# Performance work log

Hardware: AMD Instinct MI355X
Metric: run time of the kernel (lower is better)

Reference implementation:

```python
import jax, jax.numpy as jnp
import numpy as np

N = 50000      # nodes
E = 800000     # edges
IN = 256       # in_dim
D = 64         # hidden_dim per head
H = 4          # heads
OUT = 40       # out_dim (classes)
SLOPE = 0.2    # leaky relu negative slope


def _gat_conv(h, src, dst, W, al, ar, heads, dh, res=None, act=False):
    """DGL-style GATConv. h:[N,Fin], W:[Fin,heads*dh], al/ar:[heads,dh]."""
    n = h.shape[0]
    feat = (h @ W).reshape(n, heads, dh)                 # [N,H,D]
    el = jnp.sum(feat * al, axis=-1)                     # [N,H]
    er = jnp.sum(feat * ar, axis=-1)                     # [N,H]
    e = jax.nn.leaky_relu(el[src] + er[dst], SLOPE)      # [E,H]
    # segment softmax over incoming edges of each dst node
    m = jax.ops.segment_max(e, dst, num_segments=n)      # [N,H]
    ex = jnp.exp(e - m[dst])                             # [E,H]
    s = jax.ops.segment_sum(ex, dst, num_segments=n)     # [N,H]
    alpha = ex / s[dst]                                  # [E,H]
    rst = jax.ops.segment_sum(alpha[:, :, None] * feat[src], dst, num_segments=n)  # [N,H,D]
    if res is not None:
        rst = rst + res
    if act:
        rst = jax.nn.elu(rst)
    return rst


def setup_inputs():
    key = jax.random.key(0)
    ks = jax.random.split(key, 16)
    def p(k, shape, fan_in):
        return (jax.random.normal(k, shape, jnp.float32) / np.sqrt(fan_in)).astype(jnp.float32)
    inputs = jax.random.normal(ks[0], (N, IN), jnp.float32)
    src = jax.random.randint(ks[1], (E,), 0, N, dtype=jnp.int32)
    dst = jax.random.randint(ks[2], (E,), 0, N, dtype=jnp.int32)
    return {
        "inputs": inputs, "src": src, "dst": dst,
        "W0": p(ks[3], (IN, H * D), IN), "al0": p(ks[4], (H, D), D), "ar0": p(ks[5], (H, D), D),
        "W1": p(ks[6], (H * D, H * D), H * D), "al1": p(ks[7], (H, D), D), "ar1": p(ks[8], (H, D), D),
        "Wo": p(ks[9], (H * D, H * OUT), H * D), "alo": p(ks[10], (H, OUT), OUT), "aro": p(ks[11], (H, OUT), OUT),
        "res_Wo": p(ks[12], (H * D, H * OUT), H * D),
        "fc_W": p(ks[13], (IN, D), IN),
    }


def reference(inputs, src, dst, W0, al0, ar0, W1, al1, ar1, Wo, alo, aro, res_Wo, fc_W):
    # layer 0: no residual, elu activation
    h = _gat_conv(inputs, src, dst, W0, al0, ar0, H, D, res=None, act=True)
    h = h.reshape(N, H * D)
    # layer 1: identity residual (in_feats == heads*out_feats), elu
    res1 = h.reshape(N, H, D)
    h = _gat_conv(h, src, dst, W1, al1, ar1, H, D, res=res1, act=True)
    h = h.reshape(N, H * D)
    # output layer: linear residual projection, no activation, mean over heads
    res_o = (h @ res_Wo).reshape(N, H, OUT)
    logits = _gat_conv(h, src, dst, Wo, alo, aro, H, OUT, res=res_o, act=False).mean(axis=1)
    seq_fts = inputs @ fc_W
    return (logits, h, seq_fts)
```

## Files before the change

### kernel.cpp

```cpp
#include <hip/hip_runtime.h>

typedef unsigned short u16;
typedef unsigned int u32;
typedef __attribute__((ext_vector_type(8))) short short8;
typedef __attribute__((ext_vector_type(4))) float f32x4;

#define NN 50000
#define EE 800000
#define EPAD (EE + 8*NN)

__device__ __forceinline__ float b2f(u16 u){ union{float f;u32 i;}x; x.i=((u32)u)<<16; return x.f; }
__device__ __forceinline__ u16 f2b(float f){ union{float f;u32 i;}x; x.f=f; u32 i=x.i; return (u16)((i + 0x7fffu + ((i>>16)&1u))>>16); }

__global__ void k_f2b4(const float* __restrict__ x, u16* __restrict__ y, int n4){
  int i = blockIdx.x*256 + threadIdx.x;
  if (i >= n4) return;
  float4 v = ((const float4*)x)[i];
  ushort4 o; o.x=f2b(v.x); o.y=f2b(v.y); o.z=f2b(v.z); o.w=f2b(v.w);
  ((ushort4*)y)[i]=o;
}

__global__ void k_wtr(const float* __restrict__ W, u16* __restrict__ Wt, int N){
  int i = blockIdx.x*256 + threadIdx.x;
  if (i >= 256*N) return;
  int k = i / N, n = i % N;
  Wt[(size_t)n*256 + k] = f2b(W[i]);
}

__global__ void k_catWoT(const float* __restrict__ rWo, const float* __restrict__ Wo, u16* __restrict__ Bct){
  int i = blockIdx.x*256 + threadIdx.x;
  if (i >= 256*320) return;
  int k = i/320, c = i%320;
  float v = (c < 160) ? rWo[k*160 + c] : Wo[k*160 + (c-160)];
  Bct[(size_t)c*256 + k] = f2b(v);
}

__global__ void k_count(const int* __restrict__ dst, int* __restrict__ cnt){
  int i = blockIdx.x*256+threadIdx.x; if (i<EE) atomicAdd(&cnt[dst[i]],1);
}

__global__ void k_scan_blocks(const int* __restrict__ cnt, int* __restrict__ off, int* __restrict__ part, int n){
  __shared__ int ts[256];
  int t = threadIdx.x; int base = blockIdx.x*1024 + t*4;
  int c0 = (base+0<n)?((cnt[base+0]+7)&~7):0;
  int c1 = (base+1<n)?((cnt[base+1]+7)&~7):0;
  int c2 = (base+2<n)?((cnt[base+2]+7)&~7):0;
  int c3 = (base+3<n)?((cnt[base+3]+7)&~7):0;
  int s = c0+c1+c2+c3;
  ts[t]=s; __syncthreads();
  for (int d=1; d<256; d<<=1){ int v=(t>=d)?ts[t-d]:0; __syncthreads(); ts[t]+=v; __syncthreads(); }
  int ex = ts[t]-s;
  if (t==255) part[blockIdx.x]=ts[255];
  if (base+0<n) off[base+0]=ex; ex+=c0;
  if (base+1<n) off[base+1]=ex; ex+=c1;
  if (base+2<n) off[base+2]=ex; ex+=c2;
  if (base+3<n) off[base+3]=ex;
}

__global__ void k_scan_part(int* part, int nb){
  if (threadIdx.x==0 && blockIdx.x==0){ int run=0; for(int i=0;i<nb;++i){ int v=part[i]; part[i]=run; run+=v; } }
}

__global__ void k_addback(int* off, int* cur, const int* __restrict__ part, int n){
  int base = blockIdx.x*1024 + threadIdx.x*4; int p = part[blockIdx.x];
  #pragma unroll
  for (int j=0;j<4;++j) if (base+j<n){ int v = off[base+j]+p; off[base+j]=v; if (base+j<NN) cur[base+j]=v; }
}

__global__ void k_scatter(const int* __restrict__ src, const int* __restrict__ dst, int* __restrict__ cur,
                          int* __restrict__ srcs){
  int i = blockIdx.x*256+threadIdx.x; if (i>=EE) return;
  int d = dst[i]; int p = atomicAdd(&cur[d],1);
  srcs[p]=src[i];
}

template<int BN, int MODE>
__global__ __launch_bounds__(256) void k_gemm2(const u16* __restrict__ A, const u16* __restrict__ Bt,
                                               void* __restrict__ C0, void* __restrict__ C1,
                                               const float* __restrict__ AL, const float* __restrict__ AR,
                                               float* __restrict__ EL, float* __restrict__ ER,
                                               int M, int ldC){
  __shared__ u16 lds[(128+BN)*256];
  u16* As = lds;
  u16* Bs = lds + 128*256;
  const int tid = threadIdx.x;
  const int row0 = blockIdx.x * 128;
  const int n0   = blockIdx.y * BN;
  #pragma unroll
  for (int it=0; it<16; ++it){
    int slot = it*256 + tid;
    int r = slot >> 5, s = slot & 31;
    int gs = s ^ (r & 7);
    const u16* gp = A + (size_t)(row0 + r)*256 + (gs<<3);
    u16* lp = As + (size_t)(it*256 + (tid & ~63))*8;
    __builtin_amdgcn_global_load_lds((const void*)gp, (void*)lp, 16, 0, 0);
  }
  #pragma unroll
  for (int it=0; it<BN/8; ++it){
    int slot = it*256 + tid;
    int r = slot >> 5, s = slot & 31;
    int gs = s ^ (r & 7);
    const u16* gp = Bt + (size_t)(n0 + r)*256 + (gs<<3);
    u16* lp = Bs + (size_t)(it*256 + (tid & ~63))*8;
    __builtin_amdgcn_global_load_lds((const void*)gp, (void*)lp, 16, 0, 0);
  }
  __syncthreads();
  const int wave = tid >> 6, l = tid & 63;
  const int wm = wave >> 1, wn = wave & 1;
  const int lr = l & 15, lq = l >> 4;
  const int NR = BN/32;
  f32x4 acc[4][4];
  #pragma unroll
  for (int mr=0;mr<4;++mr)
    #pragma unroll
    for (int nr=0;nr<NR;++nr) acc[mr][nr]=(f32x4)0.0f;
  #pragma unroll
  for (int kk=0; kk<8; ++kk){
    short8 a[4], b[4];
    #pragma unroll
    for (int mr=0;mr<4;++mr){
      int rloc = wm*64 + mr*16 + lr;
      int byo = rloc*512 + ((kk*64 + lq*16) ^ ((rloc&7)<<4));
      a[mr] = *(const short8*)((const char*)As + byo);
    }
    #pragma unroll
    for (int nr=0;nr<NR;++nr){
      int cloc = wn*(BN/2) + nr*16 + lr;
      int byo = cloc*512 + ((kk*64 + lq*16) ^ ((cloc&7)<<4));
      b[nr] = *(const short8*)((const char*)Bs + byo);
    }
    #pragma unroll
    for (int mr=0;mr<4;++mr)
      #pragma unroll
      for (int nr=0;nr<NR;++nr)
        acc[mr][nr] = __builtin_amdgcn_mfma_f32_16x16x32_bf16(a[mr], b[nr], acc[mr][nr], 0, 0, 0);
  }
  #pragma unroll
  for (int mr=0;mr<4;++mr)
    #pragma unroll
    for (int nr=0;nr<NR;++nr)
      #pragma unroll
      for (int q=0;q<4;++q){
        int r = row0 + wm*64 + mr*16 + lq*4 + q;
        if (r < M){
          int c = n0 + wn*(BN/2) + nr*16 + lr;
          float v = acc[mr][nr][q];
          if constexpr (MODE == 0)      ((float*)C0)[(size_t)r*ldC + c] = v;
          else if constexpr (MODE == 1) ((u16*)C0)[(size_t)r*ldC + c] = f2b(v);
          else {
            if (c < 160)      ((u16*)C0)[(size_t)r*160 + c]       = f2b(v);
            else if (c < 320) ((u16*)C1)[(size_t)r*160 + (c-160)] = f2b(v);
          }
        }
      }
  if constexpr (MODE == 1){
    const int head = (n0 + wn*64) >> 6;
    float alc[4], arc[4];
    #pragma unroll
    for (int nr=0;nr<4;++nr){
      int c = n0 + wn*64 + nr*16 + lr;
      alc[nr] = AL[c]; arc[nr] = AR[c];
    }
    #pragma unroll
    for (int mr=0;mr<4;++mr)
      #pragma unroll
      for (int q=0;q<4;++q){
        float suml = acc[mr][0][q]*alc[0] + acc[mr][1][q]*alc[1] + acc[mr][2][q]*alc[2] + acc[mr][3][q]*alc[3];
        float sumr = acc[mr][0][q]*arc[0] + acc[mr][1][q]*arc[1] + acc[mr][2][q]*arc[2] + acc[mr][3][q]*arc[3];
        #pragma unroll
        for (int msk=1; msk<16; msk<<=1){ suml += __shfl_xor(suml,msk,64); sumr += __shfl_xor(sumr,msk,64); }
        int r = row0 + wm*64 + mr*16 + lq*4 + q;
        if (lr == 0 && r < M){ EL[r*4+head] = suml; ER[r*4+head] = sumr; }
      }
  }
}

__global__ void k_eler(const u16* __restrict__ feat, const float* __restrict__ al, const float* __restrict__ ar,
                       float* __restrict__ el, float* __restrict__ er, int Dh, int HD){
  int t = blockIdx.x*256 + threadIdx.x;
  int n = t >> 6; int l = t & 63;
  if (n >= NN) return;
  int h = l >> 4, s = l & 15;
  const u16* fr = feat + (size_t)n*HD + h*Dh;
  const float* alh = al + h*Dh; const float* arh = ar + h*Dh;
  float accl = 0.f, accr = 0.f;
  for (int d = s; d < Dh; d += 16){ float f = b2f(fr[d]); accl += f*alh[d]; accr += f*arh[d]; }
  #pragma unroll
  for (int m = 8; m >= 1; m >>= 1){ accl += __shfl_xor(accl, m, 64); accr += __shfl_xor(accr, m, 64); }
  if (s == 0){ el[n*4+h] = accl; er[n*4+h] = accr; }
}

__device__ __forceinline__ float4 soft_prefix(const float* __restrict__ el, float4 e4,
    const int* __restrict__ srcs, float* __restrict__ es, int o0, int o1p, int oend, int l){
  float4 m; m.x=m.y=m.z=m.w=-1e30f;
  for (int e = o0 + l; e < o1p; e += 64){
    float4 v;
    if (e < oend){
      float4 a = ((const float4*)el)[srcs[e]];
      v.x=a.x+e4.x; v.x=v.x>=0.f?v.x:0.2f*v.x;
      v.y=a.y+e4.y; v.y=v.y>=0.f?v.y:0.2f*v.y;
      v.z=a.z+e4.z; v.z=v.z>=0.f?v.z:0.2f*v.z;
      v.w=a.w+e4.w; v.w=v.w>=0.f?v.w:0.2f*v.w;
    } else { v.x=v.y=v.z=v.w=-1e30f; }
    ((float4*)es)[e] = v;
    m.x=fmaxf(m.x,v.x); m.y=fmaxf(m.y,v.y); m.z=fmaxf(m.z,v.z); m.w=fmaxf(m.w,v.w);
  }
  #pragma unroll
  for (int msk=1; msk<64; msk<<=1){
    m.x=fmaxf(m.x,__shfl_xor(m.x,msk,64)); m.y=fmaxf(m.y,__shfl_xor(m.y,msk,64));
    m.z=fmaxf(m.z,__shfl_xor(m.z,msk,64)); m.w=fmaxf(m.w,__shfl_xor(m.w,msk,64));
  }
  float4 s; s.x=s.y=s.z=s.w=0.f;
  for (int e = o0 + l; e < o1p; e += 64){
    float4 v = ((const float4*)es)[e];
    v.x=__expf(v.x-m.x); v.y=__expf(v.y-m.y); v.z=__expf(v.z-m.z); v.w=__expf(v.w-m.w);
    ((float4*)es)[e]=v;
    s.x+=v.x; s.y+=v.y; s.z+=v.z; s.w+=v.w;
  }
  #pragma unroll
  for (int msk=1; msk<64; msk<<=1){
    s.x+=__shfl_xor(s.x,msk,64); s.y+=__shfl_xor(s.y,msk,64);
    s.z+=__shfl_xor(s.z,msk,64); s.w+=__shfl_xor(s.w,msk,64);
  }
  float4 rc;
  rc.x = s.x>0.f ? 1.f/s.x : 0.f;
  rc.y = s.y>0.f ? 1.f/s.y : 0.f;
  rc.z = s.z>0.f ? 1.f/s.z : 0.f;
  rc.w = s.w>0.f ? 1.f/s.w : 0.f;
  return rc;
}

template<bool RES>
__global__ __launch_bounds__(256) void k_agg64(const u16* __restrict__ feat,
    const float* __restrict__ el, const float* __restrict__ er, float* __restrict__ es,
    const int* __restrict__ off, const int* __restrict__ cnt, const int* __restrict__ srcs,
    const u16* __restrict__ resid, float* __restrict__ outf, u16* __restrict__ outb){
  const int l = threadIdx.x & 63, w = threadIdx.x >> 6;
  const int n = blockIdx.x*4 + w;
  const int o0 = off[n], o1p = off[n+1];
  const int oend = o0 + cnt[n];
  float4 e4 = ((const float4*)er)[n];
  float4 rc4 = soft_prefix(el, e4, srcs, es, o0, o1p, oend, l);
  const int lh = l & 31;
  const int half = l >> 5;
  const int h = lh >> 3;
  const float rch = ((const float*)&rc4)[h];
  float a0=0.f,a1=0.f,a2=0.f,a3=0.f,a4=0.f,a5=0.f,a6=0.f,a7=0.f;
  for (int i = o0; i < o1p; i += 8){
    #pragma unroll
    for (int u=0; u<4; ++u){
      int e = i + u*2 + half;
      int sv = srcs[e];
      float al = es[(size_t)e*4 + h];
      short8 f = *(const short8*)(feat + (size_t)sv*256 + lh*8);
      a0 += al*b2f((u16)f[0]); a1 += al*b2f((u16)f[1]);
      a2 += al*b2f((u16)f[2]); a3 += al*b2f((u16)f[3]);
      a4 += al*b2f((u16)f[4]); a5 += al*b2f((u16)f[5]);
      a6 += al*b2f((u16)f[6]); a7 += al*b2f((u16)f[7]);
    }
  }
  a0 += __shfl_xor(a0,32,64); a1 += __shfl_xor(a1,32,64);
  a2 += __shfl_xor(a2,32,64); a3 += __shfl_xor(a3,32,64);
  a4 += __shfl_xor(a4,32,64); a5 += __shfl_xor(a5,32,64);
  a6 += __shfl_xor(a6,32,64); a7 += __shfl_xor(a7,32,64);
  if (half == 0){
    float v[8] = {a0*rch,a1*rch,a2*rch,a3*rch,a4*rch,a5*rch,a6*rch,a7*rch};
    if (RES){
      short8 r8 = *(const short8*)(resid + (size_t)n*256 + lh*8);
      #pragma unroll
      for (int j=0;j<8;++j) v[j] += b2f((u16)r8[j]);
    }
    #pragma unroll
    for (int j=0;j<8;++j) v[j] = v[j] > 0.f ? v[j] : expm1f(v[j]);
    if (outf){
      float4 q0; q0.x=v[0]; q0.y=v[1]; q0.z=v[2]; q0.w=v[3];
      float4 q1; q1.x=v[4]; q1.y=v[5]; q1.z=v[6]; q1.w=v[7];
      *(float4*)(outf + (size_t)n*256 + lh*8)     = q0;
      *(float4*)(outf + (size_t)n*256 + lh*8 + 4) = q1;
    }
    short8 ob;
    #pragma unroll
    for (int j=0;j<8;++j) ob[j] = (short)f2b(v[j]);
    *(short8*)(outb + (size_t)n*256 + lh*8) = ob;
  }
}

__global__ __launch_bounds__(256) void k_agg_out(const u16* __restrict__ feat,
    const float* __restrict__ el, const float* __restrict__ er, float* __restrict__ es,
    const int* __restrict__ off, const int* __restrict__ cnt, const int* __restrict__ srcs,
    const u16* __restrict__ reso, float* __restrict__ logits){
  __shared__ float red[4][8][20][8];
  __shared__ float fin[4][160];
  const int l = threadIdx.x & 63, w = threadIdx.x >> 6;
  const int n = blockIdx.x*4 + w;
  const int o0 = off[n], o1p = off[n+1];
  const int oend = o0 + cnt[n];
  float4 e4 = ((const float4*)er)[n];
  float4 rc4 = soft_prefix(el, e4, srcs, es, o0, o1p, oend, l);
  const int s0 = l/20,        q0 = l%20;
  const int s1 = (64+l)/20,   q1 = (64+l)%20;
  const int s2 = (128+l)/20,  q2 = (128+l)%20;
  const int h0 = q0/5, h1 = q1/5, h2 = q2/5;
  float acc0[8], acc1[8], acc2[8];
  #pragma unroll
  for (int j=0;j<8;++j){ acc0[j]=0.f; acc1[j]=0.f; acc2[j]=0.f; }
  for (int i0 = o0; i0 < o1p; i0 += 8){
    {
      int e = i0 + s0; int sv = srcs[e]; float al = es[(size_t)e*4 + h0];
      short8 f = *(const short8*)(feat + (size_t)sv*160 + q0*8);
      #pragma unroll
      for (int j=0;j<8;++j) acc0[j] += al*b2f((u16)f[j]);
    }
    {
      int e = i0 + s1; int sv = srcs[e]; float al = es[(size_t)e*4 + h1];
      short8 f = *(const short8*)(feat + (size_t)sv*160 + q1*8);
      #pragma unroll
      for (int j=0;j<8;++j) acc1[j] += al*b2f((u16)f[j]);
    }
    if (l < 32){
      int e = i0 + s2; int sv = srcs[e]; float al = es[(size_t)e*4 + h2];
      short8 f = *(const short8*)(feat + (size_t)sv*160 + q2*8);
      #pragma unroll
      for (int j=0;j<8;++j) acc2[j] += al*b2f((u16)f[j]);
    }
  }
  #pragma unroll
  for (int j=0;j<8;++j) red[w][s0][q0][j] = acc0[j];
  #pragma unroll
  for (int j=0;j<8;++j) red[w][s1][q1][j] = acc1[j];
  if (l < 32){
    #pragma unroll
    for (int j=0;j<8;++j) red[w][s2][q2][j] = acc2[j];
  }
  __syncthreads();
  if (l < 20){
    const int q = l;
    float rc = ((const float*)&rc4)[q/5];
    short8 rr = *(const short8*)(reso + (size_t)n*160 + q*8);
    #pragma unroll
    for (int j=0;j<8;++j){
      float v = red[w][0][q][j];
      #pragma unroll
      for (int s=1;s<8;++s) v += red[w][s][q][j];
      fin[w][q*8+j] = v*rc + b2f((u16)rr[j]);
    }
  }
  __syncthreads();
  if (l < 40) logits[(size_t)n*40 + l] = 0.25f*(fin[w][l]+fin[w][l+40]+fin[w][l+80]+fin[w][l+120]);
}

extern "C" void kernel_launch(void* const* d_in, const int* in_sizes, int n_in,
                              void* d_out, int out_size, void* d_ws, size_t ws_size,
                              hipStream_t stream){
  const float* inputs = (const float*)d_in[0];
  const int*   src    = (const int*)d_in[1];
  const int*   dst    = (const int*)d_in[2];
  const float* W0  = (const float*)d_in[3];
  const float* al0 = (const float*)d_in[4];
  const float* ar0 = (const float*)d_in[5];
  const float* W1  = (const float*)d_in[6];
  const float* al1 = (const float*)d_in[7];
  const float* ar1 = (const float*)d_in[8];
  const float* Wo  = (const float*)d_in[9];
  const float* alo = (const float*)d_in[10];
  const float* aro = (const float*)d_in[11];
  const float* rWo = (const float*)d_in[12];
  const float* fcW = (const float*)d_in[13];

  float* out = (float*)d_out;
  float* out_logits = out;
  float* out_h      = out + 2000000;
  float* out_seq    = out + 14800000;

  char* ws = (char*)d_ws;
  size_t o = 0;
  auto alc = [&](size_t bytes){ size_t r = o; o += (bytes + 255) & ~(size_t)255; return r; };
  size_t oXb   = alc((size_t)NN*256*2);
  size_t oFA   = alc((size_t)NN*256*2);
  size_t oFB   = alc((size_t)NN*256*2);
  size_t oEs   = alc((size_t)EPAD*4*4);
  size_t oSrcs = alc((size_t)EPAD*4);
  size_t oOff  = alc((size_t)(NN+1)*4);
  size_t oCnt  = alc((size_t)(NN+1)*4);
  size_t oCur  = alc((size_t)NN*4);
  size_t oPart = alc(64*4);
  size_t oEl   = alc((size_t)NN*4*4);
  size_t oEr   = alc((size_t)NN*4*4);
  size_t oReso = alc((size_t)NN*160*2);
  size_t oW0t  = alc(256*256*2);
  size_t oW1t  = alc(256*256*2);
  size_t oWct  = alc((size_t)384*256*2);
  size_t oFct  = alc((size_t)128*256*2);
  if (ws_size < o) return;

  u16* Xb   = (u16*)(ws + oXb);
  u16* fA   = (u16*)(ws + oFA);
  u16* fB   = (u16*)(ws + oFB);
  float* es = (float*)(ws + oEs);
  int* srcs = (int*)(ws + oSrcs);
  int* off  = (int*)(ws + oOff);
  int* cnt  = (int*)(ws + oCnt);
  int* cur  = (int*)(ws + oCur);
  int* part = (int*)(ws + oPart);
  float* el = (float*)(ws + oEl);
  float* er = (float*)(ws + oEr);
  u16* reso = (u16*)(ws + oReso);
  u16* W0t  = (u16*)(ws + oW0t);
  u16* W1t  = (u16*)(ws + oW1t);
  u16* Wct  = (u16*)(ws + oWct);
  u16* fct  = (u16*)(ws + oFct);

  k_f2b4<<<(NN*256/4 + 255)/256, 256, 0, stream>>>(inputs, Xb, NN*256/4);
  k_wtr<<<(256*256 + 255)/256, 256, 0, stream>>>(W0, W0t, 256);
  k_wtr<<<(256*256 + 255)/256, 256, 0, stream>>>(W1, W1t, 256);
  k_wtr<<<(256*64 + 255)/256, 256, 0, stream>>>(fcW, fct, 64);
  k_catWoT<<<(256*320 + 255)/256, 256, 0, stream>>>(rWo, Wo, Wct);

  hipMemsetAsync(cnt, 0, (size_t)(NN+1)*4, stream);
  hipMemsetAsync(srcs, 0, (size_t)EPAD*4, stream);
  k_count<<<(EE+255)/256, 256, 0, stream>>>(dst, cnt);
  const int NP1 = NN+1, NB = (NP1 + 1023)/1024;
  k_scan_blocks<<<NB, 256, 0, stream>>>(cnt, off, part, NP1);
  k_scan_part<<<1, 64, 0, stream>>>(part, NB);
  k_addback<<<NB, 256, 0, stream>>>(off, cur, part, NP1);
  k_scatter<<<(EE+255)/256, 256, 0, stream>>>(src, dst, cur, srcs);

  const int GX = (NN + 127)/128;
  dim3 g256(GX, 2), g320(GX, 3), g64(GX, 1);

  k_gemm2<64,0><<<g64, 256, 0, stream>>>(Xb, fct, out_seq, nullptr, nullptr, nullptr, nullptr, nullptr, NN, 64);

  k_gemm2<128,1><<<g256, 256, 0, stream>>>(Xb, W0t, fA, nullptr, al0, ar0, el, er, NN, 256);
  k_agg64<false><<<NN/4, 256, 0, stream>>>(fA, el, er, es, off, cnt, srcs, nullptr, nullptr, fB);

  k_gemm2<128,1><<<g256, 256, 0, stream>>>(fB, W1t, fA, nullptr, al1, ar1, el, er, NN, 256);
  k_agg64<true><<<NN/4, 256, 0, stream>>>(fA, el, er, es, off, cnt, srcs, fB, out_h, fB);

  k_gemm2<128,2><<<g320, 256, 0, stream>>>(fB, Wct, reso, fA, nullptr, nullptr, nullptr, nullptr, NN, 320);
  k_eler<<<(NN*64 + 255)/256, 256, 0, stream>>>(fA, alo, aro, el, er, 40, 160);
  k_agg_out<<<NN/4, 256, 0, stream>>>(fA, el, er, es, off, cnt, srcs, reso, out_logits);
}
```

Measured before the change: 512.6 us.

## Drop softmax max pass and recompute edge weights inline in aggregation

Removes the per-edge score buffer and the segment-max pass. Unnormalised exponentials of the leaky-relu scores (clamped at 60) are now computed once for the denominator and recomputed during feature aggregation, relying on softmax being invariant to shifting the scores. Padding edges are redirected to a sentinel node whose el is -1e30, so their weight becomes zero; this replaces the cnt bound checks and the memset of srcs. The aim is to cut the large es write and read traffic in every layer, at the cost of extra exp work, extra el gathers, and less numerical safety if scores are large.

```diff
diff --git a/kernel.cpp b/kernel.cpp
--- a/kernel.cpp
+++ b/kernel.cpp
@@ -11,6 +11,7 @@
 
 __device__ __forceinline__ float b2f(u16 u){ union{float f;u32 i;}x; x.i=((u32)u)<<16; return x.f; }
 __device__ __forceinline__ u16 f2b(float f){ union{float f;u32 i;}x; x.f=f; u32 i=x.i; return (u16)((i + 0x7fffu + ((i>>16)&1u))>>16); }
+__device__ __forceinline__ float pexp(float sc){ sc = sc>=0.f ? sc : 0.2f*sc; return __expf(fminf(sc,60.f)); }
 
 __global__ void k_f2b4(const float* __restrict__ x, u16* __restrict__ y, int n4){
   int i = blockIdx.x*256 + threadIdx.x;
@@ -27,8 +28,10 @@
   Wt[(size_t)n*256 + k] = f2b(W[i]);
 }
 
-__global__ void k_catWoT(const float* __restrict__ rWo, const float* __restrict__ Wo, u16* __restrict__ Bct){
+__global__ void k_catWoT(const float* __restrict__ rWo, const float* __restrict__ Wo, u16* __restrict__ Bct,
+                         float* __restrict__ el){
   int i = blockIdx.x*256 + threadIdx.x;
+  if (i < 4) el[NN*4 + i] = -1e30f;
   if (i >= 256*320) return;
   int k = i/320, c = i%320;
   float v = (c < 160) ? rWo[k*160 + c] : Wo[k*160 + (c-160)];
@@ -74,6 +77,12 @@
   srcs[p]=src[i];
 }
 
+__global__ void k_padfill(const int* __restrict__ off, const int* __restrict__ cnt, int* __restrict__ srcs){
+  int n = blockIdx.x*256+threadIdx.x; if (n>=NN) return;
+  int e = off[n]+cnt[n], e1 = off[n+1];
+  for (; e<e1; ++e) srcs[e] = NN;
+}
+
 template<int BN, int MODE>
 __global__ __launch_bounds__(256) void k_gemm2(const u16* __restrict__ A, const u16* __restrict__ Bt,
                                                void* __restrict__ C0, void* __restrict__ C1,
@@ -190,32 +199,15 @@
   if (s == 0){ el[n*4+h] = accl; er[n*4+h] = accr; }
 }
 
-__device__ __forceinline__ float4 soft_prefix(const float* __restrict__ el, float4 e4,
-    const int* __restrict__ srcs, float* __restrict__ es, int o0, int o1p, int oend, int l){
-  float4 m; m.x=m.y=m.z=m.w=-1e30f;
-  for (int e = o0 + l; e < o1p; e += 64){
-    float4 v;
-    if (e < oend){
-      float4 a = ((const float4*)el)[srcs[e]];
-      v.x=a.x+e4.x; v.x=v.x>=0.f?v.x:0.2f*v.x;
-      v.y=a.y+e4.y; v.y=v.y>=0.f?v.y:0.2f*v.y;
-      v.z=a.z+e4.z; v.z=v.z>=0.f?v.z:0.2f*v.z;
-      v.w=a.w+e4.w; v.w=v.w>=0.f?v.w:0.2f*v.w;
-    } else { v.x=v.y=v.z=v.w=-1e30f; }
-    ((float4*)es)[e] = v;
-    m.x=fmaxf(m.x,v.x); m.y=fmaxf(m.y,v.y); m.z=fmaxf(m.z,v.z); m.w=fmaxf(m.w,v.w);
-  }
-  #pragma unroll
-  for (int msk=1; msk<64; msk<<=1){
-    m.x=fmaxf(m.x,__shfl_xor(m.x,msk,64)); m.y=fmaxf(m.y,__shfl_xor(m.y,msk,64));
-    m.z=fmaxf(m.z,__shfl_xor(m.z,msk,64)); m.w=fmaxf(m.w,__shfl_xor(m.w,msk,64));
-  }
+__device__ __forceinline__ float4 rc_prefix(const float* __restrict__ el, float4 e4,
+    const int* __restrict__ srcs, int o0, int o1p, int l){
   float4 s; s.x=s.y=s.z=s.w=0.f;
   for (int e = o0 + l; e < o1p; e += 64){
-    float4 v = ((const float4*)es)[e];
-    v.x=__expf(v.x-m.x); v.y=__expf(v.y-m.y); v.z=__expf(v.z-m.z); v.w=__expf(v.w-m.w);
-    ((float4*)es)[e]=v;
-    s.x+=v.x; s.y+=v.y; s.z+=v.z; s.w+=v.w;
+    float4 a = ((const float4*)el)[srcs[e]];
+    s.x += pexp(a.x+e4.x);
+    s.y += pexp(a.y+e4.y);
+    s.z += pexp(a.z+e4.z);
+    s.w += pexp(a.w+e4.w);
   }
   #pragma unroll
   for (int msk=1; msk<64; msk<<=1){
@@ -232,31 +224,31 @@
 
 template<bool RES>
 __global__ __launch_bounds__(256) void k_agg64(const u16* __restrict__ feat,
-    const float* __restrict__ el, const float* __restrict__ er, float* __restrict__ es,
-    const int* __restrict__ off, const int* __restrict__ cnt, const int* __restrict__ srcs,
+    const float* __restrict__ el, const float* __restrict__ er,
+    const int* __restrict__ off, const int* __restrict__ srcs,
     const u16* __restrict__ resid, float* __restrict__ outf, u16* __restrict__ outb){
   const int l = threadIdx.x & 63, w = threadIdx.x >> 6;
   const int n = blockIdx.x*4 + w;
   const int o0 = off[n], o1p = off[n+1];
-  const int oend = o0 + cnt[n];
   float4 e4 = ((const float4*)er)[n];
-  float4 rc4 = soft_prefix(el, e4, srcs, es, o0, o1p, oend, l);
+  float4 rc4 = rc_prefix(el, e4, srcs, o0, o1p, l);
   const int lh = l & 31;
   const int half = l >> 5;
   const int h = lh >> 3;
   const float rch = ((const float*)&rc4)[h];
+  const float erh = ((const float*)&e4)[h];
   float a0=0.f,a1=0.f,a2=0.f,a3=0.f,a4=0.f,a5=0.f,a6=0.f,a7=0.f;
   for (int i = o0; i < o1p; i += 8){
     #pragma unroll
     for (int u=0; u<4; ++u){
       int e = i + u*2 + half;
       int sv = srcs[e];
-      float al = es[(size_t)e*4 + h];
+      float p = pexp(el[sv*4 + h] + erh);
       short8 f = *(const short8*)(feat + (size_t)sv*256 + lh*8);
-      a0 += al*b2f((u16)f[0]); a1 += al*b2f((u16)f[1]);
-      a2 += al*b2f((u16)f[2]); a3 += al*b2f((u16)f[3]);
-      a4 += al*b2f((u16)f[4]); a5 += al*b2f((u16)f[5]);
-      a6 += al*b2f((u16)f[6]); a7 += al*b2f((u16)f[7]);
+      a0 += p*b2f((u16)f[0]); a1 += p*b2f((u16)f[1]);
+      a2 += p*b2f((u16)f[2]); a3 += p*b2f((u16)f[3]);
+      a4 += p*b2f((u16)f[4]); a5 += p*b2f((u16)f[5]);
+      a6 += p*b2f((u16)f[6]); a7 += p*b2f((u16)f[7]);
     }
   }
   a0 += __shfl_xor(a0,32,64); a1 += __shfl_xor(a1,32,64);
@@ -286,42 +278,42 @@
 }
 
 __global__ __launch_bounds__(256) void k_agg_out(const u16* __restrict__ feat,
-    const float* __restrict__ el, const float* __restrict__ er, float* __restrict__ es,
-    const int* __restrict__ off, const int* __restrict__ cnt, const int* __restrict__ srcs,
+    const float* __restrict__ el, const float* __restrict__ er,
+    const int* __restrict__ off, const int* __restrict__ srcs,
     const u16* __restrict__ reso, float* __restrict__ logits){
   __shared__ float red[4][8][20][8];
   __shared__ float fin[4][160];
   const int l = threadIdx.x & 63, w = threadIdx.x >> 6;
   const int n = blockIdx.x*4 + w;
   const int o0 = off[n], o1p = off[n+1];
-  const int oend = o0 + cnt[n];
   float4 e4 = ((const float4*)er)[n];
-  float4 rc4 = soft_prefix(el, e4, srcs, es, o0, o1p, oend, l);
+  float4 rc4 = rc_prefix(el, e4, srcs, o0, o1p, l);
   const int s0 = l/20,        q0 = l%20;
   const int s1 = (64+l)/20,   q1 = (64+l)%20;
   const int s2 = (128+l)/20,  q2 = (128+l)%20;
   const int h0 = q0/5, h1 = q1/5, h2 = q2/5;
+  const float er0 = ((const float*)&e4)[h0], er1 = ((const float*)&e4)[h1], er2 = ((const float*)&e4)[h2];
   float acc0[8], acc1[8], acc2[8];
   #pragma unroll
   for (int j=0;j<8;++j){ acc0[j]=0.f; acc1[j]=0.f; acc2[j]=0.f; }
   for (int i0 = o0; i0 < o1p; i0 += 8){
     {
-      int e = i0 + s0; int sv = srcs[e]; float al = es[(size_t)e*4 + h0];
+      int e = i0 + s0; int sv = srcs[e]; float p = pexp(el[sv*4+h0] + er0);
       short8 f = *(const short8*)(feat + (size_t)sv*160 + q0*8);
       #pragma unroll
-      for (int j=0;j<8;++j) acc0[j] += al*b2f((u16)f[j]);
+      for (int j=0;j<8;++j) acc0[j] += p*b2f((u16)f[j]);
     }
     {
-      int e = i0 + s1; int sv = srcs[e]; float al = es[(size_t)e*4 + h1];
+      int e = i0 + s1; int sv = srcs[e]; float p = pexp(el[sv*4+h1] + er1);
       short8 f = *(const short8*)(feat + (size_t)sv*160 + q1*8);
       #pragma unroll
-      for (int j=0;j<8;++j) acc1[j] += al*b2f((u16)f[j]);
+      for (int j=0;j<8;++j) acc1[j] += p*b2f((u16)f[j]);
     }
     if (l < 32){
-      int e = i0 + s2; int sv = srcs[e]; float al = es[(size_t)e*4 + h2];
+      int e = i0 + s2; int sv = srcs[e]; float p = pexp(el[sv*4+h2] + er2);
       short8 f = *(const short8*)(feat + (size_t)sv*160 + q2*8);
       #pragma unroll
-      for (int j=0;j<8;++j) acc2[j] += al*b2f((u16)f[j]);
+      for (int j=0;j<8;++j) acc2[j] += p*b2f((u16)f[j]);
     }
   }
   #pragma unroll
@@ -378,13 +370,12 @@
   size_t oXb   = alc((size_t)NN*256*2);
   size_t oFA   = alc((size_t)NN*256*2);
   size_t oFB   = alc((size_t)NN*256*2);
-  size_t oEs   = alc((size_t)EPAD*4*4);
   size_t oSrcs = alc((size_t)EPAD*4);
   size_t oOff  = alc((size_t)(NN+1)*4);
   size_t oCnt  = alc((size_t)(NN+1)*4);
   size_t oCur  = alc((size_t)NN*4);
   size_t oPart = alc(64*4);
-  size_t oEl   = alc((size_t)NN*4*4);
+  size_t oEl   = alc((size_t)(NN+1)*4*4);
   size_t oEr   = alc((size_t)NN*4*4);
   size_t oReso = alc((size_t)NN*160*2);
   size_t oW0t  = alc(256*256*2);
@@ -396,7 +387,6 @@
   u16* Xb   = (u16*)(ws + oXb);
   u16* fA   = (u16*)(ws + oFA);
   u16* fB   = (u16*)(ws + oFB);
-  float* es = (float*)(ws + oEs);
   int* srcs = (int*)(ws + oSrcs);
   int* off  = (int*)(ws + oOff);
   int* cnt  = (int*)(ws + oCnt);
@@ -414,16 +404,16 @@
   k_wtr<<<(256*256 + 255)/256, 256, 0, stream>>>(W0, W0t, 256);
   k_wtr<<<(256*256 + 255)/256, 256, 0, stream>>>(W1, W1t, 256);
   k_wtr<<<(256*64 + 255)/256, 256, 0, stream>>>(fcW, fct, 64);
-  k_catWoT<<<(256*320 + 255)/256, 256, 0, stream>>>(rWo, Wo, Wct);
+  k_catWoT<<<(256*320 + 255)/256, 256, 0, stream>>>(rWo, Wo, Wct, el);
 
   hipMemsetAsync(cnt, 0, (size_t)(NN+1)*4, stream);
-  hipMemsetAsync(srcs, 0, (size_t)EPAD*4, stream);
   k_count<<<(EE+255)/256, 256, 0, stream>>>(dst, cnt);
   const int NP1 = NN+1, NB = (NP1 + 1023)/1024;
   k_scan_blocks<<<NB, 256, 0, stream>>>(cnt, off, part, NP1);
   k_scan_part<<<1, 64, 0, stream>>>(part, NB);
   k_addback<<<NB, 256, 0, stream>>>(off, cur, part, NP1);
   k_scatter<<<(EE+255)/256, 256, 0, stream>>>(src, dst, cur, srcs);
+  k_padfill<<<(NN+255)/256, 256, 0, stream>>>(off, cnt, srcs);
 
   const int GX = (NN + 127)/128;
   dim3 g256(GX, 2), g320(GX, 3), g64(GX, 1);
@@ -431,12 +421,12 @@
   k_gemm2<64,0><<<g64, 256, 0, stream>>>(Xb, fct, out_seq, nullptr, nullptr, nullptr, nullptr, nullptr, NN, 64);
 
   k_gemm2<128,1><<<g256, 256, 0, stream>>>(Xb, W0t, fA, nullptr, al0, ar0, el, er, NN, 256);
-  k_agg64<false><<<NN/4, 256, 0, stream>>>(fA, el, er, es, off, cnt, srcs, nullptr, nullptr, fB);
+  k_agg64<false><<<NN/4, 256, 0, stream>>>(fA, el, er, off, srcs, nullptr, nullptr, fB);
 
   k_gemm2<128,1><<<g256, 256, 0, stream>>>(fB, W1t, fA, nullptr, al1, ar1, el, er, NN, 256);
-  k_agg64<true><<<NN/4, 256, 0, stream>>>(fA, el, er, es, off, cnt, srcs, fB, out_h, fB);
+  k_agg64<true><<<NN/4, 256, 0, stream>>>(fA, el, er, off, srcs, fB, out_h, fB);
 
   k_gemm2<128,2><<<g320, 256, 0, stream>>>(fB, Wct, reso, fA, nullptr, nullptr, nullptr, nullptr, NN, 320);
   k_eler<<<(NN*64 + 255)/256, 256, 0, stream>>>(fA, alo, aro, el, er, 40, 160);
-  k_agg_out<<<NN/4, 256, 0, stream>>>(fA, el, er, es, off, cnt, srcs, reso, out_logits);
-}
+  k_agg_out<<<NN/4, 256, 0, stream>>>(fA, el, er, off, srcs, reso, out_logits);
+}
```

Measured after the change: 532.9 us. +4.0%, slower.
